# Optimization experiments

Measured on AMD Instinct MI355X. Metric: run time of the kernel, lower is better.

## Reference

```python
import jax, jax.numpy as jnp
import numpy as np

CHUNK = 512  # points per scan step; keeps per-step (B,CHUNK,M) dist tile ~64MB

def _nn_min_sqdist(x, y):
    """Per-point squared distance to nearest neighbor.
    x: (B,N,3), y: (B,M,3) -> (B,N). Chunked over N to avoid a full (B,N,M) matrix.
    """
    B, N, D = x.shape
    y2 = jnp.sum(y * y, axis=-1)  # (B,M)
    nchunks = N // CHUNK
    xc = x.reshape(B, nchunks, CHUNK, D).transpose(1, 0, 2, 3)  # (nchunks,B,C,D)

    def body(carry, xck):  # xck: (B,C,D)
        x2 = jnp.sum(xck * xck, axis=-1)  # (B,C)
        d = x2[:, :, None] + y2[:, None, :] - 2.0 * jnp.einsum('bcd,bmd->bcm', xck, y)
        return carry, jnp.min(d, axis=-1)  # (B,C)

    _, mins = jax.lax.scan(body, None, xc)  # (nchunks,B,C)
    return mins.transpose(1, 0, 2).reshape(B, N)


def setup_inputs() -> dict:
    key = jax.random.key(0)
    k1, k2 = jax.random.split(key)
    pred = jax.random.normal(k1, (4, 8192, 3), dtype=jnp.float32)
    gt = jax.random.normal(k2, (4, 8192, 3), dtype=jnp.float32)
    return {"pred": pred, "gt": gt}


def reference(pred, gt):
    beta, gamma, delta = 1.0, 1.0, 0.0  # ChamferLoss defaults; threshold=None, percentage=1.0
    N = pred.shape[1]
    pred2gt = _nn_min_sqdist(pred, gt)  # (B,N)
    gt2pred = _nn_min_sqdist(gt, pred)  # (B,M)
    loss = (jnp.mean(pred2gt, axis=-1)
            + jnp.mean(gt2pred, axis=-1) * (delta * N + gamma)
            + jnp.max(pred2gt, axis=-1) * beta)
    return jnp.mean(loss)
```

## Files before the change

### kernel.cpp

```cpp
#include <hip/hip_runtime.h>


typedef short  s16x8  __attribute__((ext_vector_type(8)));
typedef float  f32x16 __attribute__((ext_vector_type(16)));

#define BATCH 4
#define NPTS  8192
#define TPB   256
#define YS    4
#define YPS   (NPTS / YS)
#define STPTS 1024
#define STTILES (STPTS / 32)
#define XPB   256
#define NXC   (NPTS / XPB)

__device__ __forceinline__ unsigned int bft(float f) { return __float_as_uint(f) >> 16; }
__device__ __forceinline__ float bfv(unsigned int s) { return __uint_as_float(s << 16); }

__device__ __forceinline__ void yfrag(float a0, float a1, float a2,
                                      uint4& w0, uint4& w1) {
    const unsigned int yh0 = bft(a0), yh1 = bft(a1), yh2 = bft(a2);
    const float l0 = a0 - bfv(yh0), l1 = a1 - bfv(yh1), l2 = a2 - bfv(yh2);
    const unsigned int nh0 = bft(-2.f * bfv(yh0));
    const unsigned int nh1 = bft(-2.f * bfv(yh1));
    const unsigned int nh2 = bft(-2.f * bfv(yh2));
    const unsigned int nl0 = bft(-2.f * l0), nl1 = bft(-2.f * l1), nl2 = bft(-2.f * l2);
    const float y2 = a0 * a0 + a1 * a1 + a2 * a2;
    const unsigned int q2h = bft(y2);
    const unsigned int q2l = bft(y2 - bfv(q2h));
    w0.x = nh0 | (nh1 << 16);
    w0.y = nh2 | (nl0 << 16);
    w0.z = nl1 | (nl2 << 16);
    w0.w = nh0 | (nh1 << 16);
    w1.x = nh2 | (q2h << 16);
    w1.y = q2l;
    w1.z = 0u; w1.w = 0u;
}

__global__ __launch_bounds__(TPB, 4)
void nn_fused(const float* __restrict__ pred, const float* __restrict__ gt,
              float* __restrict__ pmin) {
    const int xc = blockIdx.x, sl = blockIdx.y, bd = blockIdx.z;
    const int b = bd >> 1, dir = bd & 1;
    const float* xp = (dir ? gt : pred) + (size_t)b * NPTS * 3;
    const float* yp = (dir ? pred : gt) + (size_t)b * NPTS * 3;

    const int t = threadIdx.x;
    const int w = t >> 6, l = t & 63;
    const int m32 = l & 31, hh = l >> 5;
    const int xbase = xc * XPB + w * 64;

    __shared__ uint4 ldsb[STTILES * 64];

    s16x8 af[2];
    float x2j[2];
    #pragma unroll
    for (int j = 0; j < 2; ++j) {
        const int xi = xbase + j * 32 + m32;
        const float c0 = xp[xi * 3], c1 = xp[xi * 3 + 1], c2 = xp[xi * 3 + 2];
        x2j[j] = c0 * c0 + c1 * c1 + c2 * c2;
        const unsigned int xh0 = bft(c0), xh1 = bft(c1), xh2 = bft(c2);
        const unsigned int xl0 = bft(c0 - bfv(xh0));
        const unsigned int xl1 = bft(c1 - bfv(xh1));
        const unsigned int xl2 = bft(c2 - bfv(xh2));
        s16x8 a;
        a[0] = (short)(hh ? xl2 : xh0);
        a[1] = (short)(hh ? 0x3F80u : xh1);
        a[2] = (short)(hh ? 0x3F80u : xh2);
        a[3] = (short)(hh ? 0u : xh0);
        a[4] = (short)(hh ? 0u : xh1);
        a[5] = (short)(hh ? 0u : xh2);
        a[6] = (short)(hh ? 0u : xl0);
        a[7] = (short)(hh ? 0u : xl1);
        af[j] = a;
    }

    f32x16 zero, mn0, mn1;
    #pragma unroll
    for (int r = 0; r < 16; ++r) { zero[r] = 0.f; mn0[r] = 3.4e38f; mn1[r] = 3.4e38f; }

    const uint4* bp = ldsb + l;

    for (int s = 0; s < 2; ++s) {
        if (s) __syncthreads();
        #pragma unroll
        for (int i = 0; i < 4; ++i) {
            const int p = i * 256 + t;
            const int pt = sl * YPS + s * STPTS + p;
            const float a0 = yp[pt * 3], a1 = yp[pt * 3 + 1], a2 = yp[pt * 3 + 2];
            uint4 q0, q1;
            yfrag(a0, a1, a2, q0, q1);
            ldsb[(p >> 5) * 64 + (p & 31)]      = q0;
            ldsb[(p >> 5) * 64 + 32 + (p & 31)] = q1;
        }
        __syncthreads();
        #pragma unroll
        for (int tp = 0; tp < STTILES; tp += 2) {
            const s16x8 bfa = __builtin_bit_cast(s16x8, bp[tp * 64]);
            const s16x8 bfb = __builtin_bit_cast(s16x8, bp[(tp + 1) * 64]);
            const f32x16 e0a = __builtin_amdgcn_mfma_f32_32x32x16_bf16(af[0], bfa, zero, 0, 0, 0);
            const f32x16 e1a = __builtin_amdgcn_mfma_f32_32x32x16_bf16(af[1], bfa, zero, 0, 0, 0);
            const f32x16 e0b = __builtin_amdgcn_mfma_f32_32x32x16_bf16(af[0], bfb, zero, 0, 0, 0);
            const f32x16 e1b = __builtin_amdgcn_mfma_f32_32x32x16_bf16(af[1], bfb, zero, 0, 0, 0);
            mn0 = __builtin_elementwise_min(mn0, e0a);
            mn1 = __builtin_elementwise_min(mn1, e1a);
            mn0 = __builtin_elementwise_min(mn0, e0b);
            mn1 = __builtin_elementwise_min(mn1, e1b);
        }
    }

    #pragma unroll
    for (int off = 16; off; off >>= 1) {
        #pragma unroll
        for (int r = 0; r < 16; ++r) {
            mn0[r] = fminf(mn0[r], __shfl_xor(mn0[r], off, 64));
            mn1[r] = fminf(mn1[r], __shfl_xor(mn1[r], off, 64));
        }
    }

    const int r = l & 15;
    const int row = (r & 3) + 8 * (r >> 2) + 4 * hh;
    float v0 = mn0[0], v1 = mn1[0];
    #pragma unroll
    for (int rr = 1; rr < 16; ++rr) {
        v0 = (r == rr) ? mn0[rr] : v0;
        v1 = (r == rr) ? mn1[rr] : v1;
    }
    const float x20 = __shfl(x2j[0], row, 64);
    const float x21 = __shfl(x2j[1], row, 64);
    const bool g1 = (l & 31) >= 16;
    const float d = fmaxf((g1 ? v1 : v0) + (g1 ? x21 : x20), 0.f);
    const int xpt = xbase + (g1 ? 32 : 0) + row;
    pmin[((size_t)bd * YS + sl) * NPTS + xpt] = d;
}

__global__ __launch_bounds__(1024)
void reduce_all(const float* __restrict__ pmin, float* __restrict__ out) {
    const int t  = threadIdx.x;
    const int bd = t >> 7;
    const int l  = t & 127;
    const float4* base = (const float4*)(pmin + (size_t)bd * YS * NPTS);
    float sum = 0.f, mx = -1.f;
    #pragma unroll
    for (int i = 0; i < NPTS / 128 / 4; ++i) {
        float4 q = base[i * 128 + l];
        #pragma unroll
        for (int s2 = 1; s2 < YS; ++s2) {
            const float4 rr = base[s2 * (NPTS / 4) + i * 128 + l];
            q.x = fminf(q.x, rr.x); q.y = fminf(q.y, rr.y);
            q.z = fminf(q.z, rr.z); q.w = fminf(q.w, rr.w);
        }
        sum += (q.x + q.y) + (q.z + q.w);
        mx = fmaxf(mx, fmaxf(fmaxf(q.x, q.y), fmaxf(q.z, q.w)));
    }
    #pragma unroll
    for (int off = 32; off; off >>= 1) {
        sum += __shfl_down(sum, off, 64);
        mx = fmaxf(mx, __shfl_down(mx, off, 64));
    }
    __shared__ float ss[16], sm[16];
    if ((t & 63) == 0) { ss[t >> 6] = sum; sm[t >> 6] = mx; }
    __syncthreads();
    if (t == 0) {
        float acc = 0.f;
        #pragma unroll
        for (int d = 0; d < 8; ++d) {
            const float S = ss[2 * d] + ss[2 * d + 1];
            const float M = fmaxf(sm[2 * d], sm[2 * d + 1]);
            acc += S * (1.f / NPTS) + ((d & 1) ? 0.f : M);
        }
        out[0] = acc * (1.f / BATCH);
    }
}

extern "C" void kernel_launch(void* const* d_in, const int* in_sizes, int n_in,
                              void* d_out, int out_size, void* d_ws, size_t ws_size,
                              hipStream_t stream) {
    const float* pred = (const float*)d_in[0];
    const float* gt   = (const float*)d_in[1];

    float* pmin = (float*)d_ws;

    dim3 g1(NXC, YS, 2 * BATCH);
    nn_fused<<<g1, TPB, 0, stream>>>(pred, gt, pmin);
    reduce_all<<<dim3(1), 1024, 0, stream>>>(pmin, (float*)d_out);
}
```

Before: 85.20 us.

## Parallelize final reduction across 64 blocks with atomics and last-block finish

Replaces the single-block reduction kernel with 64 blocks that each reduce one segment, then combine their partial sums and maxima through global atomics. The last block to finish computes the scalar output. The accumulator is zeroed by one thread of the first nn_fused block. The min-accumulation loop is also rewritten as a scalar three-way fminf per element. The goal is to cut the latency of the serial single-block tail, at the cost of atomic traffic and a last-block completion protocol.

```diff
diff --git a/kernel.cpp b/kernel.cpp
--- a/kernel.cpp
+++ b/kernel.cpp
@@ -13,6 +13,7 @@
 #define STTILES (STPTS / 32)
 #define XPB   256
 #define NXC   (NPTS / XPB)
+#define RBLK  64
 
 __device__ __forceinline__ unsigned int bft(float f) { return __float_as_uint(f) >> 16; }
 __device__ __forceinline__ float bfv(unsigned int s) { return __uint_as_float(s << 16); }
@@ -39,13 +40,15 @@
 
 __global__ __launch_bounds__(TPB, 4)
 void nn_fused(const float* __restrict__ pred, const float* __restrict__ gt,
-              float* __restrict__ pmin) {
+              float* __restrict__ pmin, unsigned int* __restrict__ accum) {
     const int xc = blockIdx.x, sl = blockIdx.y, bd = blockIdx.z;
+    const int t = threadIdx.x;
+    if (xc == 0 && sl == 0 && bd == 0 && t < 17) accum[t] = 0u;
+
     const int b = bd >> 1, dir = bd & 1;
     const float* xp = (dir ? gt : pred) + (size_t)b * NPTS * 3;
     const float* yp = (dir ? pred : gt) + (size_t)b * NPTS * 3;
 
-    const int t = threadIdx.x;
     const int w = t >> 6, l = t & 63;
     const int m32 = l & 31, hh = l >> 5;
     const int xbase = xc * XPB + w * 64;
@@ -102,10 +105,11 @@
             const f32x16 e1a = __builtin_amdgcn_mfma_f32_32x32x16_bf16(af[1], bfa, zero, 0, 0, 0);
             const f32x16 e0b = __builtin_amdgcn_mfma_f32_32x32x16_bf16(af[0], bfb, zero, 0, 0, 0);
             const f32x16 e1b = __builtin_amdgcn_mfma_f32_32x32x16_bf16(af[1], bfb, zero, 0, 0, 0);
-            mn0 = __builtin_elementwise_min(mn0, e0a);
-            mn1 = __builtin_elementwise_min(mn1, e1a);
-            mn0 = __builtin_elementwise_min(mn0, e0b);
-            mn1 = __builtin_elementwise_min(mn1, e1b);
+            #pragma unroll
+            for (int r = 0; r < 16; ++r) {
+                mn0[r] = fminf(fminf(mn0[r], e0a[r]), e0b[r]);
+                mn1[r] = fminf(fminf(mn1[r], e1a[r]), e1b[r]);
+            }
         }
     }
 
@@ -134,42 +138,49 @@
     pmin[((size_t)bd * YS + sl) * NPTS + xpt] = d;
 }
 
-__global__ __launch_bounds__(1024)
-void reduce_all(const float* __restrict__ pmin, float* __restrict__ out) {
-    const int t  = threadIdx.x;
-    const int bd = t >> 7;
-    const int l  = t & 127;
+__global__ __launch_bounds__(TPB)
+void reduce_all(const float* __restrict__ pmin, float* __restrict__ accum,
+                float* __restrict__ out) {
+    const int g = blockIdx.x, bd = g >> 3, seg = g & 7;
+    const int t = threadIdx.x;
     const float4* base = (const float4*)(pmin + (size_t)bd * YS * NPTS);
-    float sum = 0.f, mx = -1.f;
+    const int f4 = seg * 256 + t;
+    float4 q = base[f4];
     #pragma unroll
-    for (int i = 0; i < NPTS / 128 / 4; ++i) {
-        float4 q = base[i * 128 + l];
-        #pragma unroll
-        for (int s2 = 1; s2 < YS; ++s2) {
-            const float4 rr = base[s2 * (NPTS / 4) + i * 128 + l];
-            q.x = fminf(q.x, rr.x); q.y = fminf(q.y, rr.y);
-            q.z = fminf(q.z, rr.z); q.w = fminf(q.w, rr.w);
-        }
-        sum += (q.x + q.y) + (q.z + q.w);
-        mx = fmaxf(mx, fmaxf(fmaxf(q.x, q.y), fmaxf(q.z, q.w)));
+    for (int sl = 1; sl < YS; ++sl) {
+        const float4 rr = base[sl * (NPTS / 4) + f4];
+        q.x = fminf(q.x, rr.x); q.y = fminf(q.y, rr.y);
+        q.z = fminf(q.z, rr.z); q.w = fminf(q.w, rr.w);
     }
+    float s = (q.x + q.y) + (q.z + q.w);
+    float m = fmaxf(fmaxf(q.x, q.y), fmaxf(q.z, q.w));
     #pragma unroll
     for (int off = 32; off; off >>= 1) {
-        sum += __shfl_down(sum, off, 64);
-        mx = fmaxf(mx, __shfl_down(mx, off, 64));
+        s += __shfl_down(s, off, 64);
+        m = fmaxf(m, __shfl_down(m, off, 64));
     }
-    __shared__ float ss[16], sm[16];
-    if ((t & 63) == 0) { ss[t >> 6] = sum; sm[t >> 6] = mx; }
+    __shared__ float ws_[4], wm_[4];
+    if ((t & 63) == 0) { ws_[t >> 6] = s; wm_[t >> 6] = m; }
     __syncthreads();
     if (t == 0) {
-        float acc = 0.f;
-        #pragma unroll
-        for (int d = 0; d < 8; ++d) {
-            const float S = ss[2 * d] + ss[2 * d + 1];
-            const float M = fmaxf(sm[2 * d], sm[2 * d + 1]);
-            acc += S * (1.f / NPTS) + ((d & 1) ? 0.f : M);
+        s = (ws_[0] + ws_[1]) + (ws_[2] + ws_[3]);
+        m = fmaxf(fmaxf(wm_[0], wm_[1]), fmaxf(wm_[2], wm_[3]));
+        atomicAdd(&accum[bd], s);
+        atomicMax((unsigned int*)accum + 8 + bd, __float_as_uint(m));
+        __threadfence();
+        const unsigned int done = atomicAdd((unsigned int*)accum + 16, 1u);
+        if (done == RBLK - 1) {
+            float acc = 0.f;
+            #pragma unroll
+            for (int b2 = 0; b2 < BATCH; ++b2) {
+                const float s0 = atomicAdd(&accum[2 * b2], 0.f);
+                const float s1 = atomicAdd(&accum[2 * b2 + 1], 0.f);
+                const unsigned int mb =
+                    atomicMax((unsigned int*)accum + 8 + 2 * b2, 0u);
+                acc += (s0 + s1) * (1.f / NPTS) + __uint_as_float(mb);
+            }
+            out[0] = acc * (1.f / BATCH);
         }
-        out[0] = acc * (1.f / BATCH);
     }
 }
 
@@ -180,8 +191,9 @@
     const float* gt   = (const float*)d_in[1];
 
     float* pmin = (float*)d_ws;
+    float* accum = (float*)((char*)d_ws + (size_t)2 * BATCH * YS * NPTS * 4);
 
     dim3 g1(NXC, YS, 2 * BATCH);
-    nn_fused<<<g1, TPB, 0, stream>>>(pred, gt, pmin);
-    reduce_all<<<dim3(1), 1024, 0, stream>>>(pmin, (float*)d_out);
+    nn_fused<<<g1, TPB, 0, stream>>>(pred, gt, pmin, (unsigned int*)accum);
+    reduce_all<<<dim3(RBLK), TPB, 0, stream>>>(pmin, accum, (float*)d_out);
 }
```

Result: no change. 83.60 us (-1.9%).

## Fuse min/sum/max reduction into NN kernel and drop Y-slice split

Applied to the files above, without the earlier changes.

Each block now processes all 8192 target points, with 512 threads where each wave owns a single 32-point x tile, instead of splitting Y into four slices. It reduces sum and max per block directly into float2 partials. This removes the per-slice pmin buffer (about 1 MB of writes) and the single-block kernel that re-read it, leaving a tiny final reduction over 256 partials. The MFMA loop is software-pipelined so min folding overlaps the next MFMA pair. In exchange the grid shrinks to 256 blocks with fewer resident waves, and each LDS B-fragment read now feeds one x tile instead of two.

```diff
diff --git a/kernel.cpp b/kernel.cpp
--- a/kernel.cpp
+++ b/kernel.cpp
@@ -6,169 +6,172 @@
 
 #define BATCH 4
 #define NPTS  8192
-#define TPB   256
-#define YS    4
-#define YPS   (NPTS / YS)
-#define STPTS 1024
-#define STTILES (STPTS / 32)
+#define TPB   512
 #define XPB   256
 #define NXC   (NPTS / XPB)
+#define NPH   4
+#define PHPTS (NPTS / NPH)
+#define PHT   (PHPTS / 32)
 
 __device__ __forceinline__ unsigned int bft(float f) { return __float_as_uint(f) >> 16; }
 __device__ __forceinline__ float bfv(unsigned int s) { return __uint_as_float(s << 16); }
 
-__device__ __forceinline__ void yfrag(float a0, float a1, float a2,
-                                      uint4& w0, uint4& w1) {
-    const unsigned int yh0 = bft(a0), yh1 = bft(a1), yh2 = bft(a2);
-    const float l0 = a0 - bfv(yh0), l1 = a1 - bfv(yh1), l2 = a2 - bfv(yh2);
-    const unsigned int nh0 = bft(-2.f * bfv(yh0));
-    const unsigned int nh1 = bft(-2.f * bfv(yh1));
-    const unsigned int nh2 = bft(-2.f * bfv(yh2));
-    const unsigned int nl0 = bft(-2.f * l0), nl1 = bft(-2.f * l1), nl2 = bft(-2.f * l2);
-    const float y2 = a0 * a0 + a1 * a1 + a2 * a2;
-    const unsigned int q2h = bft(y2);
-    const unsigned int q2l = bft(y2 - bfv(q2h));
-    w0.x = nh0 | (nh1 << 16);
-    w0.y = nh2 | (nl0 << 16);
-    w0.z = nl1 | (nl2 << 16);
-    w0.w = nh0 | (nh1 << 16);
-    w1.x = nh2 | (q2h << 16);
-    w1.y = q2l;
-    w1.z = 0u; w1.w = 0u;
-}
-
-__global__ __launch_bounds__(TPB, 4)
+__global__ __launch_bounds__(TPB, 2)
 void nn_fused(const float* __restrict__ pred, const float* __restrict__ gt,
-              float* __restrict__ pmin) {
-    const int xc = blockIdx.x, sl = blockIdx.y, bd = blockIdx.z;
+              float2* __restrict__ partials) {
+    const int xc = blockIdx.x, bd = blockIdx.z;
     const int b = bd >> 1, dir = bd & 1;
     const float* xp = (dir ? gt : pred) + (size_t)b * NPTS * 3;
     const float* yp = (dir ? pred : gt) + (size_t)b * NPTS * 3;
 
     const int t = threadIdx.x;
-    const int w = t >> 6, l = t & 63;
+    const int wv = t >> 6, l = t & 63;
     const int m32 = l & 31, hh = l >> 5;
-    const int xbase = xc * XPB + w * 64;
 
-    __shared__ uint4 ldsb[STTILES * 64];
+    __shared__ uint4 ldsb[PHT * 64];
 
-    s16x8 af[2];
-    float x2j[2];
-    #pragma unroll
-    for (int j = 0; j < 2; ++j) {
-        const int xi = xbase + j * 32 + m32;
-        const float c0 = xp[xi * 3], c1 = xp[xi * 3 + 1], c2 = xp[xi * 3 + 2];
-        x2j[j] = c0 * c0 + c1 * c1 + c2 * c2;
+    const int xi = xc * XPB + wv * 32 + m32;
+    const float c0 = xp[xi * 3], c1 = xp[xi * 3 + 1], c2 = xp[xi * 3 + 2];
+    const float x2 = c0 * c0 + c1 * c1 + c2 * c2;
+    s16x8 af;
+    {
         const unsigned int xh0 = bft(c0), xh1 = bft(c1), xh2 = bft(c2);
         const unsigned int xl0 = bft(c0 - bfv(xh0));
         const unsigned int xl1 = bft(c1 - bfv(xh1));
         const unsigned int xl2 = bft(c2 - bfv(xh2));
-        s16x8 a;
-        a[0] = (short)(hh ? xl2 : xh0);
-        a[1] = (short)(hh ? 0x3F80u : xh1);
-        a[2] = (short)(hh ? 0x3F80u : xh2);
-        a[3] = (short)(hh ? 0u : xh0);
-        a[4] = (short)(hh ? 0u : xh1);
-        a[5] = (short)(hh ? 0u : xh2);
-        a[6] = (short)(hh ? 0u : xl0);
-        a[7] = (short)(hh ? 0u : xl1);
-        af[j] = a;
+        af[0] = (short)(hh ? xl2 : xh0);
+        af[1] = (short)(hh ? 0x3F80u : xh1);
+        af[2] = (short)(hh ? 0x3F80u : xh2);
+        af[3] = (short)(hh ? 0u : xh0);
+        af[4] = (short)(hh ? 0u : xh1);
+        af[5] = (short)(hh ? 0u : xh2);
+        af[6] = (short)(hh ? 0u : xl0);
+        af[7] = (short)(hh ? 0u : xl1);
     }
 
-    f32x16 zero, mn0, mn1;
+    f32x16 zero, mn;
     #pragma unroll
-    for (int r = 0; r < 16; ++r) { zero[r] = 0.f; mn0[r] = 3.4e38f; mn1[r] = 3.4e38f; }
+    for (int r = 0; r < 16; ++r) { zero[r] = 0.f; mn[r] = 3.4e38f; }
 
     const uint4* bp = ldsb + l;
 
-    for (int s = 0; s < 2; ++s) {
-        if (s) __syncthreads();
+#define FOLD(EA, EB)                                                                  \
+    do { _Pragma("unroll")                                                            \
+         for (int r = 0; r < 16; ++r)                                                 \
+             mn[r] = fminf(fminf(mn[r], (EA)[r]), (EB)[r]); } while (0)
+#define MFMA(BF) __builtin_amdgcn_mfma_f32_32x32x16_bf16(af, (BF), zero, 0, 0, 0)
+
+    for (int ph = 0; ph < NPH; ++ph) {
+        if (ph) __syncthreads();
         #pragma unroll
-        for (int i = 0; i < 4; ++i) {
-            const int p = i * 256 + t;
-            const int pt = sl * YPS + s * STPTS + p;
+        for (int i = 0; i < PHPTS / TPB; ++i) {
+            const int q = i * TPB + t;
+            const int pt = ph * PHPTS + q;
             const float a0 = yp[pt * 3], a1 = yp[pt * 3 + 1], a2 = yp[pt * 3 + 2];
-            uint4 q0, q1;
-            yfrag(a0, a1, a2, q0, q1);
-            ldsb[(p >> 5) * 64 + (p & 31)]      = q0;
-            ldsb[(p >> 5) * 64 + 32 + (p & 31)] = q1;
+            const unsigned int yh0 = bft(a0), yh1 = bft(a1), yh2 = bft(a2);
+            const float l0 = a0 - bfv(yh0), l1 = a1 - bfv(yh1), l2 = a2 - bfv(yh2);
+            const unsigned int nh0 = bft(-2.f * bfv(yh0));
+            const unsigned int nh1 = bft(-2.f * bfv(yh1));
+            const unsigned int nh2 = bft(-2.f * bfv(yh2));
+            const unsigned int nl0 = bft(-2.f * l0), nl1 = bft(-2.f * l1), nl2 = bft(-2.f * l2);
+            const float y2 = a0 * a0 + a1 * a1 + a2 * a2;
+            const unsigned int q2h = bft(y2);
+            const unsigned int q2l = bft(y2 - bfv(q2h));
+            uint4 w0, w1;
+            w0.x = nh0 | (nh1 << 16);
+            w0.y = nh2 | (nl0 << 16);
+            w0.z = nl1 | (nl2 << 16);
+            w0.w = nh0 | (nh1 << 16);
+            w1.x = nh2 | (q2h << 16);
+            w1.y = q2l;
+            w1.z = 0u; w1.w = 0u;
+            ldsb[(q >> 5) * 64 + (q & 31)]      = w0;
+            ldsb[(q >> 5) * 64 + 32 + (q & 31)] = w1;
         }
         __syncthreads();
-        #pragma unroll
-        for (int tp = 0; tp < STTILES; tp += 2) {
-            const s16x8 bfa = __builtin_bit_cast(s16x8, bp[tp * 64]);
-            const s16x8 bfb = __builtin_bit_cast(s16x8, bp[(tp + 1) * 64]);
-            const f32x16 e0a = __builtin_amdgcn_mfma_f32_32x32x16_bf16(af[0], bfa, zero, 0, 0, 0);
-            const f32x16 e1a = __builtin_amdgcn_mfma_f32_32x32x16_bf16(af[1], bfa, zero, 0, 0, 0);
-            const f32x16 e0b = __builtin_amdgcn_mfma_f32_32x32x16_bf16(af[0], bfb, zero, 0, 0, 0);
-            const f32x16 e1b = __builtin_amdgcn_mfma_f32_32x32x16_bf16(af[1], bfb, zero, 0, 0, 0);
-            mn0 = __builtin_elementwise_min(mn0, e0a);
-            mn1 = __builtin_elementwise_min(mn1, e1a);
-            mn0 = __builtin_elementwise_min(mn0, e0b);
-            mn1 = __builtin_elementwise_min(mn1, e1b);
+
+        f32x16 pA, pB, qA, qB;
+        {
+            const s16x8 b0 = __builtin_bit_cast(s16x8, bp[0]);
+            const s16x8 b1 = __builtin_bit_cast(s16x8, bp[64]);
+            pA = MFMA(b0); pB = MFMA(b1);
+        }
+        for (int i = 2; i < PHT - 2; i += 4) {
+            {
+                const s16x8 b0 = __builtin_bit_cast(s16x8, bp[i * 64]);
+                const s16x8 b1 = __builtin_bit_cast(s16x8, bp[(i + 1) * 64]);
+                qA = MFMA(b0); qB = MFMA(b1);
+                FOLD(pA, pB);
+            }
+            {
+                const s16x8 b0 = __builtin_bit_cast(s16x8, bp[(i + 2) * 64]);
+                const s16x8 b1 = __builtin_bit_cast(s16x8, bp[(i + 3) * 64]);
+                pA = MFMA(b0); pB = MFMA(b1);
+                FOLD(qA, qB);
+            }
+        }
+        {
+            const s16x8 b0 = __builtin_bit_cast(s16x8, bp[(PHT - 2) * 64]);
+            const s16x8 b1 = __builtin_bit_cast(s16x8, bp[(PHT - 1) * 64]);
+            qA = MFMA(b0); qB = MFMA(b1);
+            FOLD(pA, pB);
+            FOLD(qA, qB);
         }
     }
+#undef MFMA
+#undef FOLD
 
     #pragma unroll
-    for (int off = 16; off; off >>= 1) {
+    for (int off = 16; off; off >>= 1)
         #pragma unroll
-        for (int r = 0; r < 16; ++r) {
-            mn0[r] = fminf(mn0[r], __shfl_xor(mn0[r], off, 64));
-            mn1[r] = fminf(mn1[r], __shfl_xor(mn1[r], off, 64));
-        }
-    }
+        for (int r = 0; r < 16; ++r)
+            mn[r] = fminf(mn[r], __shfl_xor(mn[r], off, 64));
 
     const int r = l & 15;
     const int row = (r & 3) + 8 * (r >> 2) + 4 * hh;
-    float v0 = mn0[0], v1 = mn1[0];
+    float v = mn[0];
     #pragma unroll
-    for (int rr = 1; rr < 16; ++rr) {
-        v0 = (r == rr) ? mn0[rr] : v0;
-        v1 = (r == rr) ? mn1[rr] : v1;
+    for (int rr = 1; rr < 16; ++rr) v = (r == rr) ? mn[rr] : v;
+    const float x2s = __shfl(x2, row, 64);
+    const bool valid = (l & 31) < 16;
+    const float d = valid ? fmaxf(v + x2s, 0.f) : 0.f;
+
+    float s = d, m = valid ? d : -1.f;
+    #pragma unroll
+    for (int off = 32; off; off >>= 1) {
+        s += __shfl_xor(s, off, 64);
+        m = fmaxf(m, __shfl_xor(m, off, 64));
     }
-    const float x20 = __shfl(x2j[0], row, 64);
-    const float x21 = __shfl(x2j[1], row, 64);
-    const bool g1 = (l & 31) >= 16;
-    const float d = fmaxf((g1 ? v1 : v0) + (g1 ? x21 : x20), 0.f);
-    const int xpt = xbase + (g1 ? 32 : 0) + row;
-    pmin[((size_t)bd * YS + sl) * NPTS + xpt] = d;
+    __shared__ float ws_[8], wm_[8];
+    if (l == 0) { ws_[wv] = s; wm_[wv] = m; }
+    __syncthreads();
+    if (t == 0) {
+        float bs = 0.f, bm = -1.f;
+        #pragma unroll
+        for (int i = 0; i < 8; ++i) { bs += ws_[i]; bm = fmaxf(bm, wm_[i]); }
+        partials[bd * NXC + xc] = make_float2(bs, bm);
+    }
 }
 
-__global__ __launch_bounds__(1024)
-void reduce_all(const float* __restrict__ pmin, float* __restrict__ out) {
-    const int t  = threadIdx.x;
-    const int bd = t >> 7;
-    const int l  = t & 127;
-    const float4* base = (const float4*)(pmin + (size_t)bd * YS * NPTS);
-    float sum = 0.f, mx = -1.f;
+__global__ __launch_bounds__(256)
+void reduce_all(const float2* __restrict__ partials, float* __restrict__ out) {
+    const int t = threadIdx.x;
+    const float2 p = partials[t];
+    float s = p.x, m = p.y;
     #pragma unroll
-    for (int i = 0; i < NPTS / 128 / 4; ++i) {
-        float4 q = base[i * 128 + l];
-        #pragma unroll
-        for (int s2 = 1; s2 < YS; ++s2) {
-            const float4 rr = base[s2 * (NPTS / 4) + i * 128 + l];
-            q.x = fminf(q.x, rr.x); q.y = fminf(q.y, rr.y);
-            q.z = fminf(q.z, rr.z); q.w = fminf(q.w, rr.w);
-        }
-        sum += (q.x + q.y) + (q.z + q.w);
-        mx = fmaxf(mx, fmaxf(fmaxf(q.x, q.y), fmaxf(q.z, q.w)));
+    for (int off = 16; off; off >>= 1) {
+        s += __shfl_xor(s, off, 64);
+        m = fmaxf(m, __shfl_xor(m, off, 64));
     }
-    #pragma unroll
-    for (int off = 32; off; off >>= 1) {
-        sum += __shfl_down(sum, off, 64);
-        mx = fmaxf(mx, __shfl_down(mx, off, 64));
-    }
-    __shared__ float ss[16], sm[16];
-    if ((t & 63) == 0) { ss[t >> 6] = sum; sm[t >> 6] = mx; }
+    __shared__ float s8[8], m8[8];
+    if ((t & 31) == 0) { s8[t >> 5] = s; m8[t >> 5] = m; }
     __syncthreads();
     if (t == 0) {
         float acc = 0.f;
         #pragma unroll
-        for (int d = 0; d < 8; ++d) {
-            const float S = ss[2 * d] + ss[2 * d + 1];
-            const float M = fmaxf(sm[2 * d], sm[2 * d + 1]);
-            acc += S * (1.f / NPTS) + ((d & 1) ? 0.f : M);
-        }
+        for (int b2 = 0; b2 < BATCH; ++b2)
+            acc += (s8[2 * b2] + s8[2 * b2 + 1]) * (1.f / NPTS)
+                 + m8[2 * b2];
         out[0] = acc * (1.f / BATCH);
     }
 }
@@ -179,9 +182,9 @@
     const float* pred = (const float*)d_in[0];
     const float* gt   = (const float*)d_in[1];
 
-    float* pmin = (float*)d_ws;
+    float2* partials = (float2*)d_ws;
 
-    dim3 g1(NXC, YS, 2 * BATCH);
-    nn_fused<<<g1, TPB, 0, stream>>>(pred, gt, pmin);
-    reduce_all<<<dim3(1), 1024, 0, stream>>>(pmin, (float*)d_out);
+    dim3 g1(NXC, 1, 2 * BATCH);
+    nn_fused<<<g1, TPB, 0, stream>>>(pred, gt, partials);
+    reduce_all<<<dim3(1), 256, 0, stream>>>(partials, (float*)d_out);
 }
```

Result: faster. 76.29 us (-10.5%).
